# Optimization experiments

Measured on AMD Instinct MI355X. Metric: run time of the kernel, lower is better.

## Reference

```python
import jax, jax.numpy as jnp
import numpy as np

TOP_K = 2  # num_active_experts


def setup_inputs() -> dict:
    key = jax.random.key(0)
    k1, k2, k3 = jax.random.split(key, 3)
    N, D, E = 16384, 1024, 8
    x = jax.random.normal(k1, (N, D), dtype=jnp.float32)
    router_w = jax.random.normal(k2, (E, D), dtype=jnp.float32) * (1.0 / np.sqrt(D))
    router_b = jnp.zeros((E,), dtype=jnp.float32)
    expert_w = jax.random.normal(k3, (E, D, D), dtype=jnp.float32) * (1.0 / np.sqrt(D))
    expert_b = jnp.zeros((E, D), dtype=jnp.float32)
    return {"x": x, "router_w": router_w, "router_b": router_b,
            "expert_w": expert_w, "expert_b": expert_b}


def reference(x, router_w, router_b, expert_w, expert_b):
    E = router_w.shape[0]
    # Router: softmax over experts, pick top-k, renormalize
    logits = x @ router_w.T + router_b                      # [N, E]
    probs = jax.nn.softmax(logits, axis=-1)                 # [N, E]
    top_p, top_i = jax.lax.top_k(probs, TOP_K)              # [N, K]
    top_p = top_p / jnp.sum(top_p, axis=-1, keepdims=True)  # renormalized gates
    # Dense combine weights: [N, E], zero for non-selected experts
    combine = jnp.sum(jax.nn.one_hot(top_i, E, dtype=x.dtype) * top_p[..., None], axis=1)
    # All-expert outputs, then weighted combine (vectorized dispatch/combine)
    y = jnp.einsum('nd,eod->neo', x, expert_w) + expert_b   # [N, E, O]
    out = jnp.einsum('neo,ne->no', y, combine)              # [N, O]
    return out
```

## Files before the change

kernel.cpp:

```cpp
#include <hip/hip_runtime.h>
#include <hip/hip_bf16.h>


constexpr int DIMS = 1024;
constexpr int NE   = 8;
constexpr int ROUTER_BLOCKS = 1024;
constexpr int WCONV_BLOCKS  = NE * DIMS * DIMS / (8 * 256);

typedef __attribute__((ext_vector_type(8))) short short8;
typedef __attribute__((ext_vector_type(4))) short short4_t;
typedef __attribute__((ext_vector_type(4))) float f32x4;

__device__ __forceinline__ float b2f(unsigned short u) {
  union { unsigned int i; float f; } x; x.i = ((unsigned)u) << 16; return x.f;
}
__device__ __forceinline__ short f2bs(float f) {
  __hip_bfloat16 h = __float2bfloat16(f);
  return *(short*)&h;
}

__global__ __launch_bounds__(256) void prep_kernel(
    const float* __restrict__ x, const float* __restrict__ rw,
    const float* __restrict__ rb, const float* __restrict__ ew,
    __hip_bfloat16* __restrict__ xb, __hip_bfloat16* __restrict__ wb,
    int* __restrict__ counts, int* __restrict__ entries,
    float* __restrict__ gates, int n_tok) {
  const int tid = threadIdx.x;

  if ((int)blockIdx.x >= ROUTER_BLOCKS) {
    unsigned g = (unsigned)(blockIdx.x - ROUTER_BLOCKS) * 256 + tid;
    int l  = g & 63;
    int kc = (g >> 6) & 31;
    int nb = (g >> 11) & 63;
    int e  = g >> 17;
    int row = nb * 16 + (l & 15);
    int kb  = kc * 32 + ((l >> 4) << 3);
    const float4* src = (const float4*)(ew + ((size_t)e << 20) + (size_t)row * DIMS + kb);
    float4 a = src[0], b = src[1];
    union { __hip_bfloat16 h[8]; float4 f; } u;
    u.h[0] = __float2bfloat16(a.x); u.h[1] = __float2bfloat16(a.y);
    u.h[2] = __float2bfloat16(a.z); u.h[3] = __float2bfloat16(a.w);
    u.h[4] = __float2bfloat16(b.x); u.h[5] = __float2bfloat16(b.y);
    u.h[6] = __float2bfloat16(b.z); u.h[7] = __float2bfloat16(b.w);
    ((float4*)wb)[g] = u.f;
    return;
  }

  __shared__ float s_rw[NE * DIMS];
  __shared__ int s_cnt[NE], s_base[NE];
  __shared__ int s_e[32];
  __shared__ float s_g[32];
  __shared__ int s_pos[32];

  const float4* rw4g = (const float4*)rw;
  float4* s4 = (float4*)s_rw;
  for (int i = tid; i < NE * DIMS / 4; i += 256) s4[i] = rw4g[i];
  if (tid < NE) s_cnt[tid] = 0;
  __syncthreads();

  const float4* s_rw4 = (const float4*)s_rw;
  const int wave = tid >> 6, lane = tid & 63;
  for (int i = 0; i < 4; ++i) {
    int t = blockIdx.x * 16 + wave * 4 + i;
    const float4* xr = (const float4*)(x + (size_t)t * DIMS);
    short4_t* xw = (short4_t*)(xb + (size_t)t * DIMS);
    float a[NE];
#pragma unroll
    for (int e = 0; e < NE; ++e) a[e] = 0.f;
#pragma unroll
    for (int j = 0; j < 4; ++j) {
      float4 v = xr[lane + j * 64];
      short4_t p;
      p[0] = f2bs(v.x); p[1] = f2bs(v.y); p[2] = f2bs(v.z); p[3] = f2bs(v.w);
      xw[lane + j * 64] = p;
#pragma unroll
      for (int e = 0; e < NE; ++e) {
        float4 w = s_rw4[e * 256 + lane + j * 64];
        a[e] = fmaf(v.x, w.x, fmaf(v.y, w.y, fmaf(v.z, w.z, fmaf(v.w, w.w, a[e]))));
      }
    }
#pragma unroll
    for (int off = 32; off > 0; off >>= 1) {
#pragma unroll
      for (int e = 0; e < NE; ++e) a[e] += __shfl_xor(a[e], off, 64);
    }
    if (lane == 0) {
      float l[NE];
#pragma unroll
      for (int e = 0; e < NE; ++e) l[e] = a[e] + rb[e];
      int e0 = 0;
#pragma unroll
      for (int e = 1; e < NE; ++e) if (l[e] > l[e0]) e0 = e;
      int e1 = (e0 == 0) ? 1 : 0;
#pragma unroll
      for (int e = 0; e < NE; ++e) if (e != e0 && l[e] > l[e1]) e1 = e;
      float r = expf(l[e1] - l[e0]);
      float g0 = 1.f / (1.f + r);
      float g1 = 1.f - g0;
      int ai = (wave * 4 + i) * 2;
      int p0 = atomicAdd(&s_cnt[e0], 1);
      int p1 = atomicAdd(&s_cnt[e1], 1);
      s_e[ai] = e0; s_g[ai] = g0; s_pos[ai] = p0;
      s_e[ai + 1] = e1; s_g[ai + 1] = g1; s_pos[ai + 1] = p1;
    }
  }
  __syncthreads();
  if (tid < NE) s_base[tid] = atomicAdd(&counts[tid], s_cnt[tid]);
  __syncthreads();
  if (tid < 32) {
    int e = s_e[tid];
    int p = s_base[e] + s_pos[tid];
    int tok = blockIdx.x * 16 + (tid >> 1);
    entries[e * n_tok + p] = (tok << 1) | (tid & 1);
    gates[e * n_tok + p] = s_g[tid];
  }
}

__global__ __launch_bounds__(256, 2) void moe_gemm(
    const __hip_bfloat16* __restrict__ xb, const __hip_bfloat16* __restrict__ wb,
    const float* __restrict__ eb, const int* __restrict__ counts,
    const int* __restrict__ entries, const float* __restrict__ gates,
    __hip_bfloat16* __restrict__ y, int n_tok) {
  int e = -1, rt = 0, cnt = 0, acc_t = 0;
#pragma unroll
  for (int i = 0; i < NE; ++i) {
    int c = counts[i];
    int t = (c + 127) >> 7;
    if (e < 0 && (int)blockIdx.y < acc_t + t) { e = i; rt = (int)blockIdx.y - acc_t; cnt = c; }
    acc_t += t;
  }
  if (e < 0) return;

  const int tid = threadIdx.x;
  const int lane = tid & 63, wave = tid >> 6;
  const int row0 = rt * 128;
  const int n0 = blockIdx.x * 256;
  const int wm = (wave & 1) * 64, wn = (wave >> 1) * 128;
  const int fr = lane & 15, quad = lane >> 4;

  const short8* ap[4];
#pragma unroll
  for (int mb = 0; mb < 4; ++mb) {
    int gr = row0 + wm + mb * 16 + fr;
    int ent = (gr < cnt) ? entries[e * n_tok + gr] : 0;
    ap[mb] = (const short8*)(xb + (size_t)(ent >> 1) * DIMS) + quad;
  }

  const short8* wb8 = (const short8*)wb;
  const size_t bbase = ((((size_t)e * 64 + ((n0 + wn) >> 4)) * 32) << 6) + lane;

  f32x4 acc[4][8] = {};

#pragma unroll 2
  for (int kc = 0; kc < 32; ++kc) {
    short8 af[4], bf[8];
#pragma unroll
    for (int mb = 0; mb < 4; ++mb) af[mb] = ap[mb][kc * 4];
#pragma unroll
    for (int nt = 0; nt < 8; ++nt) bf[nt] = wb8[bbase + ((size_t)nt << 11) + (kc << 6)];
#pragma unroll
    for (int mt = 0; mt < 4; ++mt)
#pragma unroll
      for (int nt = 0; nt < 8; ++nt)
        acc[mt][nt] = __builtin_amdgcn_mfma_f32_16x16x32_bf16(af[mt], bf[nt], acc[mt][nt], 0, 0, 0);
  }

  float bias[8];
#pragma unroll
  for (int nt = 0; nt < 8; ++nt) bias[nt] = eb[e * DIMS + n0 + wn + nt * 16 + fr];
#pragma unroll
  for (int mt = 0; mt < 4; ++mt) {
#pragma unroll
    for (int r = 0; r < 4; ++r) {
      int m = wm + mt * 16 + quad * 4 + r;
      int gr = row0 + m;
      if (gr < cnt) {
        int ent = entries[e * n_tok + gr];
        float g = gates[e * n_tok + gr];
        __hip_bfloat16* yp = y + (size_t)ent * DIMS + n0 + wn + fr;
#pragma unroll
        for (int nt = 0; nt < 8; ++nt)
          yp[nt * 16] = __float2bfloat16(g * (acc[mt][nt][r] + bias[nt]));
      }
    }
  }
}

__global__ __launch_bounds__(256) void combine_kernel(const __hip_bfloat16* __restrict__ y,
                                                      float* __restrict__ out) {
  size_t idx = (size_t)blockIdx.x * 256 + threadIdx.x;
  size_t n = idx >> 7;
  int c = (int)(idx & 127) << 3;
  short8 v0 = *(const short8*)(y + (n * 2) * DIMS + c);
  short8 v1 = *(const short8*)(y + (n * 2 + 1) * DIMS + c);
  float4 o0, o1;
  o0.x = b2f((unsigned short)v0[0]) + b2f((unsigned short)v1[0]);
  o0.y = b2f((unsigned short)v0[1]) + b2f((unsigned short)v1[1]);
  o0.z = b2f((unsigned short)v0[2]) + b2f((unsigned short)v1[2]);
  o0.w = b2f((unsigned short)v0[3]) + b2f((unsigned short)v1[3]);
  o1.x = b2f((unsigned short)v0[4]) + b2f((unsigned short)v1[4]);
  o1.y = b2f((unsigned short)v0[5]) + b2f((unsigned short)v1[5]);
  o1.z = b2f((unsigned short)v0[6]) + b2f((unsigned short)v1[6]);
  o1.w = b2f((unsigned short)v0[7]) + b2f((unsigned short)v1[7]);
  float* op = out + n * DIMS + c;
  ((float4*)op)[0] = o0;
  ((float4*)op)[1] = o1;
}

extern "C" void kernel_launch(void* const* d_in, const int* in_sizes, int n_in,
                              void* d_out, int out_size, void* d_ws, size_t ws_size,
                              hipStream_t stream) {
  const float* x  = (const float*)d_in[0];
  const float* rw = (const float*)d_in[1];
  const float* rb = (const float*)d_in[2];
  const float* ew = (const float*)d_in[3];
  const float* eb = (const float*)d_in[4];
  float* out = (float*)d_out;
  const int n_tok = in_sizes[0] / DIMS;

  char* ws = (char*)d_ws;
  size_t off = 0;
  int* counts = (int*)ws;                      off += 256;
  __hip_bfloat16* xb = (__hip_bfloat16*)(ws + off); off += (size_t)n_tok * DIMS * 2;
  __hip_bfloat16* wb = (__hip_bfloat16*)(ws + off); off += (size_t)NE * DIMS * DIMS * 2;
  int*   entries = (int*)(ws + off);           off += (size_t)NE * n_tok * 4;
  float* gates   = (float*)(ws + off);         off += (size_t)NE * n_tok * 4;
  __hip_bfloat16* y = (__hip_bfloat16*)(ws + off); off += (size_t)n_tok * 2 * DIMS * 2;
  if (ws_size < off) return;

  hipMemsetAsync(counts, 0, 256, stream);
  prep_kernel<<<ROUTER_BLOCKS + WCONV_BLOCKS, 256, 0, stream>>>(
      x, rw, rb, ew, xb, wb, counts, entries, gates, n_tok);
  dim3 g(DIMS / 256, 2 * n_tok / 128 + NE);
  moe_gemm<<<g, 256, 0, stream>>>(xb, wb, eb, counts, entries, gates, y, n_tok);
  combine_kernel<<<(unsigned)((size_t)n_tok * DIMS / 8 / 256), 256, 0, stream>>>(y, out);
}
```

Measured before the change: 321.2 us.

## Stage gathered tokens in LDS, shrink GEMM tile, remap blocks per XCD, deterministic scan

Replaces the global atomic expert-slot allocation with per-block counts, a single-block prefix scan and a scatter kernel, which makes entry order deterministic and removes the memset. The GEMM now uses 128x128 tiles and stages the gathered A rows into swizzled LDS with global_load_lds, so waves share the A tile instead of each re-reading it from global memory. Occupancy goes from 2 to 4 blocks per CU, and blocks are remapped so that each XCD handles a contiguous group of row tiles, aiming for better L2 reuse. The cost is two extra kernel launches, two barriers per k-step, and no double buffering of the LDS tile. RT_PER_XCD is fixed at 33, which hard-codes the row-tile capacity.

```diff
diff --git a/kernel.cpp b/kernel.cpp
--- a/kernel.cpp
+++ b/kernel.cpp
@@ -6,10 +6,14 @@
 constexpr int NE   = 8;
 constexpr int ROUTER_BLOCKS = 1024;
 constexpr int WCONV_BLOCKS  = NE * DIMS * DIMS / (8 * 256);
+constexpr int RT_PER_XCD = 33;
 
 typedef __attribute__((ext_vector_type(8))) short short8;
 typedef __attribute__((ext_vector_type(4))) short short4_t;
 typedef __attribute__((ext_vector_type(4))) float f32x4;
+
+typedef const __attribute__((address_space(1))) void* gp_t;
+typedef __attribute__((address_space(3))) void* sp_t;
 
 __device__ __forceinline__ float b2f(unsigned short u) {
   union { unsigned int i; float f; } x; x.i = ((unsigned)u) << 16; return x.f;
@@ -23,8 +27,8 @@
     const float* __restrict__ x, const float* __restrict__ rw,
     const float* __restrict__ rb, const float* __restrict__ ew,
     __hip_bfloat16* __restrict__ xb, __hip_bfloat16* __restrict__ wb,
-    int* __restrict__ counts, int* __restrict__ entries,
-    float* __restrict__ gates, int n_tok) {
+    int* __restrict__ blk_cnt, int* __restrict__ tmp_meta,
+    float* __restrict__ tmp_gate, int n_tok) {
   const int tid = threadIdx.x;
 
   if ((int)blockIdx.x >= ROUTER_BLOCKS) {
@@ -47,7 +51,7 @@
   }
 
   __shared__ float s_rw[NE * DIMS];
-  __shared__ int s_cnt[NE], s_base[NE];
+  __shared__ int s_cnt[NE];
   __shared__ int s_e[32];
   __shared__ float s_g[32];
   __shared__ int s_pos[32];
@@ -105,69 +109,113 @@
     }
   }
   __syncthreads();
-  if (tid < NE) s_base[tid] = atomicAdd(&counts[tid], s_cnt[tid]);
-  __syncthreads();
+  if (tid < NE) blk_cnt[blockIdx.x * NE + tid] = s_cnt[tid];
   if (tid < 32) {
-    int e = s_e[tid];
-    int p = s_base[e] + s_pos[tid];
-    int tok = blockIdx.x * 16 + (tid >> 1);
-    entries[e * n_tok + p] = (tok << 1) | (tid & 1);
-    gates[e * n_tok + p] = s_g[tid];
-  }
-}
-
-__global__ __launch_bounds__(256, 2) void moe_gemm(
+    int s = blockIdx.x * 32 + tid;
+    tmp_meta[s] = s_e[tid] | (s_pos[tid] << 3);
+    tmp_gate[s] = s_g[tid];
+  }
+}
+
+__global__ __launch_bounds__(512) void scan_kernel(
+    const int* __restrict__ blk_cnt, int* __restrict__ blk_base,
+    int* __restrict__ counts) {
+  const int e = threadIdx.x >> 6, lane = threadIdx.x & 63;
+  int running = 0;
+  for (int c = 0; c < ROUTER_BLOCKS / 64; ++c) {
+    int v = blk_cnt[(c * 64 + lane) * NE + e];
+    int incl = v;
+#pragma unroll
+    for (int off = 1; off < 64; off <<= 1) {
+      int t = __shfl_up(incl, off, 64);
+      if (lane >= off) incl += t;
+    }
+    blk_base[(c * 64 + lane) * NE + e] = running + incl - v;
+    running += __shfl(incl, 63, 64);
+  }
+  if (lane == 0) counts[e] = running;
+}
+
+__global__ __launch_bounds__(256) void scatter_kernel(
+    const int* __restrict__ tmp_meta, const float* __restrict__ tmp_gate,
+    const int* __restrict__ blk_base, int* __restrict__ entries,
+    float* __restrict__ gates, int n_tok) {
+  int s = blockIdx.x * 256 + threadIdx.x;
+  int meta = tmp_meta[s];
+  int e = meta & 7, pos = meta >> 3;
+  int p = blk_base[(s >> 5) * NE + e] + pos;
+  entries[e * n_tok + p] = ((s >> 1) << 1) | (s & 1);
+  gates[e * n_tok + p] = tmp_gate[s];
+}
+
+__global__ __launch_bounds__(256, 4) void moe_gemm(
     const __hip_bfloat16* __restrict__ xb, const __hip_bfloat16* __restrict__ wb,
     const float* __restrict__ eb, const int* __restrict__ counts,
     const int* __restrict__ entries, const float* __restrict__ gates,
     __hip_bfloat16* __restrict__ y, int n_tok) {
+  const int xcd = blockIdx.x & 7;
+  const int j = blockIdx.x >> 3;
+  const int ct = j & 7;
+  const int virt = xcd * RT_PER_XCD + (j >> 3);
+
   int e = -1, rt = 0, cnt = 0, acc_t = 0;
 #pragma unroll
   for (int i = 0; i < NE; ++i) {
     int c = counts[i];
     int t = (c + 127) >> 7;
-    if (e < 0 && (int)blockIdx.y < acc_t + t) { e = i; rt = (int)blockIdx.y - acc_t; cnt = c; }
+    if (e < 0 && virt < acc_t + t) { e = i; rt = virt - acc_t; cnt = c; }
     acc_t += t;
   }
   if (e < 0) return;
+
+  __shared__ __hip_bfloat16 As[128 * 32];
 
   const int tid = threadIdx.x;
   const int lane = tid & 63, wave = tid >> 6;
   const int row0 = rt * 128;
-  const int n0 = blockIdx.x * 256;
-  const int wm = (wave & 1) * 64, wn = (wave >> 1) * 128;
+  const int n0 = ct * 128;
+
+  const int srow = tid >> 2;
+  const int kcs = (tid & 3) ^ (srow & 3);
+  const int kcol = kcs * 8;
+  int gr0 = row0 + srow, gr1 = row0 + srow + 64;
+  int ent0 = (gr0 < cnt) ? entries[e * n_tok + gr0] : 0;
+  int ent1 = (gr1 < cnt) ? entries[e * n_tok + gr1] : 0;
+  const __hip_bfloat16* ap0 = xb + (size_t)(ent0 >> 1) * DIMS + kcol;
+  const __hip_bfloat16* ap1 = xb + (size_t)(ent1 >> 1) * DIMS + kcol;
+
+  const int wm = (wave & 1) * 64, wn = (wave >> 1) * 64;
   const int fr = lane & 15, quad = lane >> 4;
-
-  const short8* ap[4];
-#pragma unroll
-  for (int mb = 0; mb < 4; ++mb) {
-    int gr = row0 + wm + mb * 16 + fr;
-    int ent = (gr < cnt) ? entries[e * n_tok + gr] : 0;
-    ap[mb] = (const short8*)(xb + (size_t)(ent >> 1) * DIMS) + quad;
-  }
+  const int swo = (quad ^ (fr & 3)) * 8;
 
   const short8* wb8 = (const short8*)wb;
-  const size_t bbase = ((((size_t)e * 64 + ((n0 + wn) >> 4)) * 32) << 6) + lane;
-
-  f32x4 acc[4][8] = {};
-
-#pragma unroll 2
-  for (int kc = 0; kc < 32; ++kc) {
-    short8 af[4], bf[8];
-#pragma unroll
-    for (int mb = 0; mb < 4; ++mb) af[mb] = ap[mb][kc * 4];
-#pragma unroll
-    for (int nt = 0; nt < 8; ++nt) bf[nt] = wb8[bbase + ((size_t)nt << 11) + (kc << 6)];
+  const size_t bbase = (((size_t)e * 64 + ((n0 + wn) >> 4)) * 32) * 64 + lane;
+
+  f32x4 acc[4][4] = {};
+
+  for (int ks = 0; ks < 32; ++ks) {
+    __builtin_amdgcn_global_load_lds((gp_t)(ap0 + ks * 32), (sp_t)(As + tid * 8), 16, 0, 0);
+    __builtin_amdgcn_global_load_lds((gp_t)(ap1 + ks * 32), (sp_t)(As + (tid + 256) * 8), 16, 0, 0);
+    short8 bf[4];
+#pragma unroll
+    for (int nt = 0; nt < 4; ++nt)
+      bf[nt] = wb8[bbase + (size_t)nt * 2048 + ks * 64];
+    __syncthreads();
+    short8 af[4];
 #pragma unroll
     for (int mt = 0; mt < 4; ++mt)
-#pragma unroll
-      for (int nt = 0; nt < 8; ++nt)
+      af[mt] = *(const short8*)&As[(wm + mt * 16 + fr) * 32 + swo];
+#pragma unroll
+    for (int mt = 0; mt < 4; ++mt)
+#pragma unroll
+      for (int nt = 0; nt < 4; ++nt)
         acc[mt][nt] = __builtin_amdgcn_mfma_f32_16x16x32_bf16(af[mt], bf[nt], acc[mt][nt], 0, 0, 0);
-  }
-
-  float bias[8];
-#pragma unroll
-  for (int nt = 0; nt < 8; ++nt) bias[nt] = eb[e * DIMS + n0 + wn + nt * 16 + fr];
+    __syncthreads();
+  }
+
+  float bias[4];
+#pragma unroll
+  for (int nt = 0; nt < 4; ++nt) bias[nt] = eb[e * DIMS + n0 + wn + nt * 16 + fr];
 #pragma unroll
   for (int mt = 0; mt < 4; ++mt) {
 #pragma unroll
@@ -179,7 +227,7 @@
         float g = gates[e * n_tok + gr];
         __hip_bfloat16* yp = y + (size_t)ent * DIMS + n0 + wn + fr;
 #pragma unroll
-        for (int nt = 0; nt < 8; ++nt)
+        for (int nt = 0; nt < 4; ++nt)
           yp[nt * 16] = __float2bfloat16(g * (acc[mt][nt][r] + bias[nt]));
       }
     }
@@ -217,21 +265,28 @@
   const float* eb = (const float*)d_in[4];
   float* out = (float*)d_out;
   const int n_tok = in_sizes[0] / DIMS;
+  const int n_slot = 2 * n_tok;
 
   char* ws = (char*)d_ws;
   size_t off = 0;
   int* counts = (int*)ws;                      off += 256;
+  int* blk_cnt = (int*)(ws + off);             off += (size_t)ROUTER_BLOCKS * NE * 4;
+  int* blk_base = (int*)(ws + off);            off += (size_t)ROUTER_BLOCKS * NE * 4;
+  int* tmp_meta = (int*)(ws + off);            off += (size_t)n_slot * 4;
+  float* tmp_gate = (float*)(ws + off);        off += (size_t)n_slot * 4;
   __hip_bfloat16* xb = (__hip_bfloat16*)(ws + off); off += (size_t)n_tok * DIMS * 2;
   __hip_bfloat16* wb = (__hip_bfloat16*)(ws + off); off += (size_t)NE * DIMS * DIMS * 2;
   int*   entries = (int*)(ws + off);           off += (size_t)NE * n_tok * 4;
   float* gates   = (float*)(ws + off);         off += (size_t)NE * n_tok * 4;
-  __hip_bfloat16* y = (__hip_bfloat16*)(ws + off); off += (size_t)n_tok * 2 * DIMS * 2;
+  __hip_bfloat16* y = (__hip_bfloat16*)(ws + off); off += (size_t)n_slot * DIMS * 2;
   if (ws_size < off) return;
 
-  hipMemsetAsync(counts, 0, 256, stream);
   prep_kernel<<<ROUTER_BLOCKS + WCONV_BLOCKS, 256, 0, stream>>>(
-      x, rw, rb, ew, xb, wb, counts, entries, gates, n_tok);
-  dim3 g(DIMS / 256, 2 * n_tok / 128 + NE);
-  moe_gemm<<<g, 256, 0, stream>>>(xb, wb, eb, counts, entries, gates, y, n_tok);
+      x, rw, rb, ew, xb, wb, blk_cnt, tmp_meta, tmp_gate, n_tok);
+  scan_kernel<<<1, 512, 0, stream>>>(blk_cnt, blk_base, counts);
+  scatter_kernel<<<n_slot / 256, 256, 0, stream>>>(
+      tmp_meta, tmp_gate, blk_base, entries, gates, n_tok);
+  moe_gemm<<<8 * RT_PER_XCD * 8, 256, 0, stream>>>(
+      xb, wb, eb, counts, entries, gates, y, n_tok);
   combine_kernel<<<(unsigned)((size_t)n_tok * DIMS / 8 / 256), 256, 0, stream>>>(y, out);
 }
```

Measured after the change: 273.0 us. -15.0%, faster.
